# Optimization experiments

Hardware: AMD Instinct MI355X
Metric: run time of the kernel (lower is better)

Reference implementation:

```python
import jax, jax.numpy as jnp
import numpy as np

EMB = 300; TOWERS = 6; LAYERS = 4; EPS = 1e-5; F_OUT = EMB // TOWERS  # 50
N_NODES = 3000; N_EDGES = 9000; N_GRAPHS = 64
NODE_VOCAB = 16; EDGE_VOCAB = 4


def _bn(x, g, b, m, v):
    # eval-mode BatchNorm1d with running stats
    return (x - m) * jax.lax.rsqrt(v + EPS) * g + b


def _forward(node_emb, edge_emb, W_edge, b_edge, W_pre, b_pre, W_post, b_post,
             W_lin, b_lin, bn_gamma, bn_beta, bn_mean, bn_var,
             head_w0, head_b0, gn0_gamma, gn0_beta, gn0_mean, gn0_var,
             head_w1, head_b1, gn1_gamma, gn1_beta, gn1_mean, gn1_var,
             head_w2, head_b2, x, edge_index, edge_attr, batch, num_graphs):
    N = x.shape[0]
    src, dst = edge_index[0], edge_index[1]
    h = node_emb[x]            # [N, D] node encoder (categorical embedding)
    e = edge_emb[edge_attr]    # [E, D] edge encoder
    cnt = jax.ops.segment_sum(jnp.ones(src.shape, h.dtype), dst, num_segments=N)
    deg = jnp.maximum(cnt, 1.0)
    log_deg = jnp.log(deg + 1.0)
    avg_log = jnp.mean(jnp.log(cnt + 1.0))  # PNA avg_deg['log'] of degree histogram
    amp = (log_deg / avg_log)[:, None, None]
    att = (avg_log / log_deg)[:, None, None]
    has_nb = (cnt > 0)[:, None, None]
    degc = deg[:, None, None]

    h_list = [h]
    for l in range(LAYERS):
        eproj = e @ W_edge[l] + b_edge[l]                        # [E, D]
        hcat = jnp.concatenate([h[dst], h[src], eproj], -1)      # [E, 3D] = [x_i, x_j, e]
        m = jnp.einsum('ef,tfd->etd', hcat, W_pre[l]) + b_pre[l]  # [E, T, D] per-tower pre-MLP
        s = jax.ops.segment_sum(m, dst, num_segments=N)
        mean = s / degc
        mn = jnp.where(has_nb, jax.ops.segment_min(m, dst, num_segments=N), 0.0)
        mx = jnp.where(has_nb, jax.ops.segment_max(m, dst, num_segments=N), 0.0)
        var = jax.ops.segment_sum(m * m, dst, num_segments=N) / degc - mean * mean
        std = jnp.sqrt(jax.nn.relu(var) + EPS)
        agg = jnp.concatenate([mean, mn, mx, std], -1)           # [N, T, 4D]
        agg = jnp.concatenate([agg, agg * amp, agg * att], -1)   # [N, T, 12D] scalers
        x_rep = jnp.broadcast_to(h[:, None, :], (N, TOWERS, EMB))
        post_in = jnp.concatenate([x_rep, agg], -1)              # [N, T, 13D]
        out = jnp.einsum('ntf,tfo->nto', post_in, W_post[l]) + b_post[l]  # [N, T, F_OUT]
        out = out.reshape(N, EMB) @ W_lin[l] + b_lin[l]
        out = _bn(out, bn_gamma[l], bn_beta[l], bn_mean[l], bn_var[l])
        if l < LAYERS - 1:
            out = jax.nn.relu(out)  # dropout is identity in eval mode
        h_list.append(out)
        h = out
    # JK='sum' exactly as in the original forward: sums h_list[0..num_layer-1]
    node_rep = h_list[0]
    for l in range(1, LAYERS):
        node_rep = node_rep + h_list[l]
    g = jax.ops.segment_sum(node_rep, batch, num_segments=num_graphs)  # global_add_pool
    g = jax.nn.relu(_bn(g @ head_w0 + head_b0, gn0_gamma, gn0_beta, gn0_mean, gn0_var))
    g = jax.nn.relu(_bn(g @ head_w1 + head_b1, gn1_gamma, gn1_beta, gn1_mean, gn1_var))
    return g @ head_w2 + head_b2


def setup_inputs() -> dict:
    key = jax.random.key(0)
    ks = jax.random.split(key, 16)
    D, T, L = EMB, TOWERS, LAYERS
    def rn(k, shape, s=0.05):
        return jax.random.normal(k, shape, dtype=jnp.float32) * s
    return {
        'x': jax.random.randint(ks[0], (N_NODES,), 0, NODE_VOCAB, dtype=jnp.int32),
        'edge_index': jax.random.randint(ks[1], (2, N_EDGES), 0, N_NODES, dtype=jnp.int32),
        'edge_attr': jax.random.randint(ks[2], (N_EDGES,), 0, EDGE_VOCAB, dtype=jnp.int32),
        'batch': jnp.sort(jax.random.randint(ks[3], (N_NODES,), 0, N_GRAPHS, dtype=jnp.int32)),
        'num_graphs': N_GRAPHS,
        'node_emb': rn(ks[4], (NODE_VOCAB, D), 1.0),
        'edge_emb': rn(ks[5], (EDGE_VOCAB, D), 1.0),
        'W_edge': rn(ks[6], (L, D, D)), 'b_edge': jnp.zeros((L, D), jnp.float32),
        'W_pre': rn(ks[7], (L, T, 3 * D, D)), 'b_pre': jnp.zeros((L, T, D), jnp.float32),
        'W_post': rn(ks[8], (L, T, 13 * D, F_OUT)), 'b_post': jnp.zeros((L, T, F_OUT), jnp.float32),
        'W_lin': rn(ks[9], (L, D, D)), 'b_lin': jnp.zeros((L, D), jnp.float32),
        'bn_gamma': jnp.ones((L, D), jnp.float32), 'bn_beta': jnp.zeros((L, D), jnp.float32),
        'bn_mean': jnp.zeros((L, D), jnp.float32), 'bn_var': jnp.ones((L, D), jnp.float32),
        'head_w0': rn(ks[10], (D, 2 * D)), 'head_b0': jnp.zeros((2 * D,), jnp.float32),
        'gn0_gamma': jnp.ones((2 * D,), jnp.float32), 'gn0_beta': jnp.zeros((2 * D,), jnp.float32),
        'gn0_mean': jnp.zeros((2 * D,), jnp.float32), 'gn0_var': jnp.ones((2 * D,), jnp.float32),
        'head_w1': rn(ks[11], (2 * D, D)), 'head_b1': jnp.zeros((D,), jnp.float32),
        'gn1_gamma': jnp.ones((D,), jnp.float32), 'gn1_beta': jnp.zeros((D,), jnp.float32),
        'gn1_mean': jnp.zeros((D,), jnp.float32), 'gn1_var': jnp.ones((D,), jnp.float32),
        'head_w2': rn(ks[12], (D, 1)), 'head_b2': jnp.zeros((1,), jnp.float32),
    }


def reference(x, edge_index, edge_attr, batch, num_graphs,
              node_emb, edge_emb, W_edge, b_edge, W_pre, b_pre, W_post, b_post,
              W_lin, b_lin, bn_gamma, bn_beta, bn_mean, bn_var,
              head_w0, head_b0, gn0_gamma, gn0_beta, gn0_mean, gn0_var,
              head_w1, head_b1, gn1_gamma, gn1_beta, gn1_mean, gn1_var,
              head_w2, head_b2):
    return _forward(node_emb, edge_emb, W_edge, b_edge, W_pre, b_pre, W_post, b_post,
                    W_lin, b_lin, bn_gamma, bn_beta, bn_mean, bn_var,
                    head_w0, head_b0, gn0_gamma, gn0_beta, gn0_mean, gn0_var,
                    head_w1, head_b1, gn1_gamma, gn1_beta, gn1_mean, gn1_var,
                    head_w2, head_b2, x, edge_index, edge_attr, batch, num_graphs)
```

## Files before the change

### kernel.cpp

```cpp
#include <hip/hip_runtime.h>
#include <math.h>

#define NN 3000
#define NE 9000
#define NG 64
#define D 300
#define NT 6
#define FO 50
#define EPSV 1e-5f
#define NB1 3900

__global__ void k_hist(const int* __restrict__ dst, int* __restrict__ cnt) {
    int e = blockIdx.x * blockDim.x + threadIdx.x;
    if (e < NE) atomicAdd(&cnt[dst[e]], 1);
}

__global__ __launch_bounds__(1024) void k_scan(
    const int* __restrict__ cnt, int* __restrict__ row_ptr, int* __restrict__ tmp_ptr,
    float* __restrict__ degf, float* __restrict__ ampv, float* __restrict__ attv) {
    __shared__ int s_part[1024];
    __shared__ float s_log[1024];
    int tid = threadIdx.x;
    int base = tid * 3;
    int c0 = 0, c1 = 0, c2 = 0; float lg = 0.f;
    if (base + 0 < NN) { c0 = cnt[base + 0]; lg += logf((float)c0 + 1.f); }
    if (base + 1 < NN) { c1 = cnt[base + 1]; lg += logf((float)c1 + 1.f); }
    if (base + 2 < NN) { c2 = cnt[base + 2]; lg += logf((float)c2 + 1.f); }
    s_part[tid] = c0 + c1 + c2;
    s_log[tid] = lg;
    __syncthreads();
    for (int off = 1; off < 1024; off <<= 1) {
        int v = (tid >= off) ? s_part[tid - off] : 0;
        __syncthreads();
        s_part[tid] += v;
        __syncthreads();
    }
    for (int off = 512; off > 0; off >>= 1) {
        if (tid < off) s_log[tid] += s_log[tid + off];
        __syncthreads();
    }
    float avg = s_log[0] / (float)NN;
    int run = (tid > 0) ? s_part[tid - 1] : 0;
    int cs[3] = {c0, c1, c2};
    for (int i = 0; i < 3; i++) {
        int n = base + i;
        if (n < NN) {
            row_ptr[n] = run; tmp_ptr[n] = run;
            int cc = cs[i];
            float dd = (float)(cc > 0 ? cc : 1);
            degf[n] = dd;
            float ld = logf(dd + 1.f);
            ampv[n] = ld / avg;
            attv[n] = avg / ld;
            run += cc;
        }
    }
    if (tid == 1023) row_ptr[NN] = s_part[1023];
}

__global__ void k_fill(const int* __restrict__ src, const int* __restrict__ dst,
                       const int* __restrict__ attr, int* __restrict__ tmp_ptr,
                       int2* __restrict__ edge_dat) {
    int e = blockIdx.x * blockDim.x + threadIdx.x;
    if (e < NE) {
        int d = dst[e];
        int p = atomicAdd(&tmp_ptr[d], 1);
        edge_dat[p] = make_int2(src[e], attr[e]);
    }
}

__global__ void k_embed(const int* __restrict__ x, const float* __restrict__ node_emb,
                        float* __restrict__ h, float* __restrict__ rep) {
    int i = blockIdx.x * blockDim.x + threadIdx.x;
    if (i < NN * D) {
        int n = i / D, d = i - n * D;
        float v = node_emb[x[n] * D + d];
        h[i] = v; rep[i] = v;
    }
}

__global__ void k_pack1(const float* __restrict__ W_pre, const float* __restrict__ W_post,
                        int l, float* __restrict__ Bp) {
    int idx = blockIdx.x * blockDim.x + threadIdx.x;
    if (idx >= 300 * NB1) return;
    int f = idx / NB1, j = idx - f * NB1;
    float v;
    if (j < 3600) {
        int s = j / 1800, r = j - s * 1800;
        int t = r / 300, d = r - t * 300;
        v = W_pre[(((size_t)(l * NT + t) * 900) + s * 300 + f) * 300 + d];
    } else {
        int jj = j - 3600;
        int t = jj / FO, o = jj - t * FO;
        v = W_post[((size_t)(l * NT + t) * 3900 + f) * FO + o];
    }
    Bp[idx] = v;
}

__global__ void k_packpost(const float* __restrict__ W_post, int l, float* __restrict__ Bp) {
    int idx = blockIdx.x * blockDim.x + threadIdx.x;
    if (idx >= NT * 1200 * 160) return;
    int t = idx / 192000, r = idx - t * 192000;
    int f = r / 160, c = r - f * 160;
    float v = 0.f;
    if (c < 150) {
        int k = c / FO, o = c - k * FO;
        v = W_post[((size_t)(l * NT + t) * 3900 + 300 + k * 1200 + f) * FO + o];
    }
    Bp[idx] = v;
}

__global__ void k_ep4(const float* __restrict__ edge_emb, const float* __restrict__ W_edge,
                      const float* __restrict__ b_edge, int l, float* __restrict__ ep4) {
    int idx = blockIdx.x * blockDim.x + threadIdx.x;
    if (idx >= 4 * 300) return;
    int a = idx / 300, f = idx - a * 300;
    float s = b_edge[l * 300 + f];
    for (int k = 0; k < 300; k++)
        s = fmaf(edge_emb[a * 300 + k], W_edge[((size_t)l * 300 + k) * 300 + f], s);
    ep4[idx] = s;
}

__global__ void k_ep_proj(const float* __restrict__ ep4, const float* __restrict__ W_pre,
                          const float* __restrict__ b_pre, int l, float* __restrict__ Ep) {
    int idx = blockIdx.x * blockDim.x + threadIdx.x;
    if (idx >= 4 * 1800) return;
    int a = idx / 1800, c = idx - a * 1800;
    int t = c / 300, d = c - t * 300;
    float s = b_pre[(l * NT + t) * 300 + d];
    for (int f = 0; f < 300; f++)
        s = fmaf(ep4[a * 300 + f], W_pre[(((size_t)(l * NT + t) * 900) + 600 + f) * 300 + d], s);
    Ep[idx] = s;
}

__global__ void k_pack_lin(const float* __restrict__ W_lin, const float* __restrict__ b_lin,
                           const float* __restrict__ gam, const float* __restrict__ bet,
                           const float* __restrict__ mu, const float* __restrict__ var,
                           int l, float* __restrict__ Wf, float* __restrict__ bf) {
    int idx = blockIdx.x * blockDim.x + threadIdx.x;
    if (idx >= 300 * 300) return;
    int f = idx / 300, j = idx - f * 300;
    float s = gam[l * 300 + j] * rsqrtf(var[l * 300 + j] + EPSV);
    Wf[idx] = W_lin[((size_t)l * 300 + f) * 300 + j] * s;
    if (f == 0) bf[j] = (b_lin[l * 300 + j] - mu[l * 300 + j]) * s + bet[l * 300 + j];
}

template <int EPI>
__global__ __launch_bounds__(256) void k_gemm(
    const float* __restrict__ A, int lda,
    const float* __restrict__ B, int ldb,
    float* __restrict__ C, int ldc,
    int M, int N, int K,
    const float* __restrict__ bias, float* __restrict__ rep,
    const float* __restrict__ gam, const float* __restrict__ bet,
    const float* __restrict__ mu, const float* __restrict__ var) {
    constexpr int BM = 64, BN = 64, BK = 16, LAS = BM + 4;
    __shared__ float As[BK * LAS];
    __shared__ float Bs[BK * BN];
    int tid = threadIdx.x;
    int tx = tid & 15, ty = tid >> 4;
    int bm = blockIdx.y * BM, bn = blockIdx.x * BN;
    int arow = tid >> 2;
    int akq = (tid & 3) * 4;
    int bj = tid & 63, bk0 = tid >> 6;
    float acc[4][4] = {};
    for (int k0 = 0; k0 < K; k0 += BK) {
        {
            float4 av = make_float4(0.f, 0.f, 0.f, 0.f);
            int grow = bm + arow;
            if (grow < M) {
                int gk = k0 + akq;
                if (gk + 3 < K) {
                    av = *(const float4*)&A[(size_t)grow * lda + gk];
                } else {
                    float t0 = (gk + 0 < K) ? A[(size_t)grow * lda + gk + 0] : 0.f;
                    float t1 = (gk + 1 < K) ? A[(size_t)grow * lda + gk + 1] : 0.f;
                    float t2 = (gk + 2 < K) ? A[(size_t)grow * lda + gk + 2] : 0.f;
                    float t3 = (gk + 3 < K) ? A[(size_t)grow * lda + gk + 3] : 0.f;
                    av = make_float4(t0, t1, t2, t3);
                }
            }
            As[(akq + 0) * LAS + arow] = av.x;
            As[(akq + 1) * LAS + arow] = av.y;
            As[(akq + 2) * LAS + arow] = av.z;
            As[(akq + 3) * LAS + arow] = av.w;
        }
        #pragma unroll
        for (int it = 0; it < 4; ++it) {
            int k = bk0 + it * 4;
            int gk = k0 + k, gj = bn + bj;
            float v = 0.f;
            if (gk < K && gj < N) v = B[(size_t)gk * ldb + gj];
            Bs[k * BN + bj] = v;
        }
        __syncthreads();
        #pragma unroll
        for (int kk = 0; kk < BK; ++kk) {
            float4 a = *(const float4*)&As[kk * LAS + ty * 4];
            float4 b = *(const float4*)&Bs[kk * BN + tx * 4];
            float ar[4] = {a.x, a.y, a.z, a.w};
            float br[4] = {b.x, b.y, b.z, b.w};
            #pragma unroll
            for (int i = 0; i < 4; i++)
                #pragma unroll
                for (int j = 0; j < 4; j++)
                    acc[i][j] = fmaf(ar[i], br[j], acc[i][j]);
        }
        __syncthreads();
    }
    #pragma unroll
    for (int i = 0; i < 4; i++) {
        int r = bm + ty * 4 + i;
        if (r >= M) continue;
        #pragma unroll
        for (int j = 0; j < 4; j++) {
            int c = bn + tx * 4 + j;
            if (c >= N) continue;
            float v = acc[i][j];
            if (EPI == 1) {
                v += bias[c];
                v = fmaxf(v, 0.f);
                C[(size_t)r * ldc + c] = v;
                rep[(size_t)r * ldc + c] += v;
            } else if (EPI == 2) {
                v += bias[c];
                v = (v - mu[c]) * rsqrtf(var[c] + EPSV) * gam[c] + bet[c];
                v = fmaxf(v, 0.f);
                C[(size_t)r * ldc + c] = v;
            } else {
                C[(size_t)r * ldc + c] = v;
            }
        }
    }
}

__global__ __launch_bounds__(256) void k_gemm1(const float* __restrict__ A,
                                               const float* __restrict__ B,
                                               float* __restrict__ C) {
    constexpr int BM = 128, BN = 128, BK = 16, LAS = BM + 4;
    constexpr int M = 3000, N = NB1, K = 300;
    __shared__ float As[BK * LAS];
    __shared__ float Bs[BK * BN];
    int tid = threadIdx.x;
    int tx = tid & 15, ty = tid >> 4;
    int bm = blockIdx.y * BM, bn = blockIdx.x * BN;
    float acc[8][8] = {};
    for (int k0 = 0; k0 < K; k0 += BK) {
        #pragma unroll
        for (int it = 0; it < 2; ++it) {
            int i = tid + it * 256;
            int row = i >> 2, kq = (i & 3) * 4;
            int grow = bm + row, gk = k0 + kq;
            float4 av = make_float4(0.f, 0.f, 0.f, 0.f);
            if (grow < M && gk < K) av = *(const float4*)&A[(size_t)grow * 300 + gk];
            As[(kq + 0) * LAS + row] = av.x;
            As[(kq + 1) * LAS + row] = av.y;
            As[(kq + 2) * LAS + row] = av.z;
            As[(kq + 3) * LAS + row] = av.w;
        }
        #pragma unroll
        for (int it = 0; it < 2; ++it) {
            int i = tid + it * 256;
            int k = i >> 5, c = (i & 31) * 4;
            int gk = k0 + k, gj = bn + c;
            float4 bv = make_float4(0.f, 0.f, 0.f, 0.f);
            if (gk < K && gj < N) bv = *(const float4*)&B[(size_t)gk * N + gj];
            *(float4*)&Bs[k * BN + c] = bv;
        }
        __syncthreads();
        #pragma unroll
        for (int kk = 0; kk < BK; ++kk) {
            float a[8], b[8];
            *(float4*)&a[0] = *(const float4*)&As[kk * LAS + ty * 8];
            *(float4*)&a[4] = *(const float4*)&As[kk * LAS + ty * 8 + 4];
            *(float4*)&b[0] = *(const float4*)&Bs[kk * BN + tx * 8];
            *(float4*)&b[4] = *(const float4*)&Bs[kk * BN + tx * 8 + 4];
            #pragma unroll
            for (int i = 0; i < 8; i++)
                #pragma unroll
                for (int j = 0; j < 8; j++)
                    acc[i][j] = fmaf(a[i], b[j], acc[i][j]);
        }
        __syncthreads();
    }
    int r0 = bm + ty * 8, c0 = bn + tx * 8;
    #pragma unroll
    for (int i = 0; i < 8; i++) {
        int r = r0 + i;
        if (r >= M) break;
        if (c0 + 8 <= N) {
            float4 v0 = make_float4(acc[i][0], acc[i][1], acc[i][2], acc[i][3]);
            float4 v1 = make_float4(acc[i][4], acc[i][5], acc[i][6], acc[i][7]);
            *(float4*)&C[(size_t)r * N + c0] = v0;
            *(float4*)&C[(size_t)r * N + c0 + 4] = v1;
        } else {
            #pragma unroll
            for (int j = 0; j < 8; j++)
                if (c0 + j < N) C[(size_t)r * N + c0 + j] = acc[i][j];
        }
    }
}

__global__ __launch_bounds__(256) void k_gemmp(const float* __restrict__ agg,
                                               const float* __restrict__ Bp,
                                               float* __restrict__ P) {
    constexpr int BM = 64, BN = 160, BK = 16, LAS = BM + 4, KC = 240;
    __shared__ float As[BK * LAS];
    __shared__ float Bs[BK * BN];
    int z = blockIdx.z;
    int t = z % 6, kc = z / 6;
    const float* A = agg + t * 1200 + kc * KC;
    const float* B = Bp + t * 192000 + kc * KC * 160;
    float* C = P + (size_t)z * 480000;
    int tid = threadIdx.x;
    int tx = tid & 15, ty = tid >> 4;
    int bm = blockIdx.y * BM;
    float acc[4][10] = {};
    for (int k0 = 0; k0 < KC; k0 += BK) {
        {
            int row = tid >> 2, kq = (tid & 3) * 4;
            int grow = bm + row;
            float4 av = make_float4(0.f, 0.f, 0.f, 0.f);
            if (grow < 3000) av = *(const float4*)&A[(size_t)grow * 7200 + k0 + kq];
            As[(kq + 0) * LAS + row] = av.x;
            As[(kq + 1) * LAS + row] = av.y;
            As[(kq + 2) * LAS + row] = av.z;
            As[(kq + 3) * LAS + row] = av.w;
        }
        #pragma unroll
        for (int it = 0; it < 3; ++it) {
            int i = tid + it * 256;
            if (i < 640) {
                int k = i / 40, c = (i - k * 40) * 4;
                *(float4*)&Bs[k * BN + c] = *(const float4*)&B[(size_t)(k0 + k) * 160 + c];
            }
        }
        __syncthreads();
        #pragma unroll
        for (int kk = 0; kk < BK; ++kk) {
            float a[4], b[10];
            *(float4*)&a[0] = *(const float4*)&As[kk * LAS + ty * 4];
            #pragma unroll
            for (int j = 0; j < 10; j++) b[j] = Bs[kk * BN + tx * 10 + j];
            #pragma unroll
            for (int i = 0; i < 4; i++)
                #pragma unroll
                for (int j = 0; j < 10; j++)
                    acc[i][j] = fmaf(a[i], b[j], acc[i][j]);
        }
        __syncthreads();
    }
    int r0 = bm + ty * 4, c0 = tx * 10;
    #pragma unroll
    for (int i = 0; i < 4; i++) {
        int r = r0 + i;
        if (r >= 3000) break;
        #pragma unroll
        for (int j = 0; j < 10; j++)
            C[(size_t)r * 160 + c0 + j] = acc[i][j];
    }
}

__global__ __launch_bounds__(256) void k_agg(
    const float* __restrict__ HH, const float* __restrict__ Ep,
    const int* __restrict__ row_ptr, const int2* __restrict__ edge_dat,
    const float* __restrict__ degf, const int* __restrict__ xv, int use_vocab,
    float* __restrict__ agg) {
    int n = blockIdx.x;
    int e0 = row_ptr[n], e1 = row_ptr[n + 1];
    int cnt = e1 - e0;
    float cntf = (float)cnt;
    float deg = degf[n];
    float inv_deg = 1.f / deg;
    int nrow = use_vocab ? xv[n] : n;
    const float* hdrow = HH + (size_t)nrow * NB1;
    for (int c4 = threadIdx.x; c4 < 450; c4 += 256) {
        int c = c4 * 4;
        float sx = 0.f, sy = 0.f, sz = 0.f, sw = 0.f;
        float qx = 0.f, qy = 0.f, qz = 0.f, qw = 0.f;
        float mnx = INFINITY, mny = INFINITY, mnz = INFINITY, mnw = INFINITY;
        float mxx = -INFINITY, mxy = -INFINITY, mxz = -INFINITY, mxw = -INFINITY;
        for (int e = e0; e < e1; ++e) {
            int2 sa = edge_dat[e];
            int srow = use_vocab ? xv[sa.x] : sa.x;
            float4 hv = *(const float4*)&HH[(size_t)srow * NB1 + 1800 + c];
            float4 ev = *(const float4*)&Ep[(size_t)sa.y * 1800 + c];
            float vx = hv.x + ev.x, vy = hv.y + ev.y, vz = hv.z + ev.z, vw = hv.w + ev.w;
            sx += vx; sy += vy; sz += vz; sw += vw;
            qx = fmaf(vx, vx, qx); qy = fmaf(vy, vy, qy);
            qz = fmaf(vz, vz, qz); qw = fmaf(vw, vw, qw);
            mnx = fminf(mnx, vx); mny = fminf(mny, vy);
            mnz = fminf(mnz, vz); mnw = fminf(mnw, vw);
            mxx = fmaxf(mxx, vx); mxy = fmaxf(mxy, vy);
            mxz = fmaxf(mxz, vz); mxw = fmaxf(mxw, vw);
        }
        float4 hd = *(const float4*)&hdrow[c];
        float4 mean, mnv, mxv, stdv;
        {
            mean.x = (cntf * hd.x + sx) * inv_deg;
            mean.y = (cntf * hd.y + sy) * inv_deg;
            mean.z = (cntf * hd.z + sz) * inv_deg;
            mean.w = (cntf * hd.w + sw) * inv_deg;
            if (cnt > 0) {
                mnv.x = hd.x + mnx; mnv.y = hd.y + mny; mnv.z = hd.z + mnz; mnv.w = hd.w + mnw;
                mxv.x = hd.x + mxx; mxv.y = hd.y + mxy; mxv.z = hd.z + mxz; mxv.w = hd.w + mxw;
            } else {
                mnv = make_float4(0.f, 0.f, 0.f, 0.f);
                mxv = make_float4(0.f, 0.f, 0.f, 0.f);
            }
            float vrx = (cntf * hd.x * hd.x + 2.f * hd.x * sx + qx) * inv_deg - mean.x * mean.x;
            float vry = (cntf * hd.y * hd.y + 2.f * hd.y * sy + qy) * inv_deg - mean.y * mean.y;
            float vrz = (cntf * hd.z * hd.z + 2.f * hd.z * sz + qz) * inv_deg - mean.z * mean.z;
            float vrw = (cntf * hd.w * hd.w + 2.f * hd.w * sw + qw) * inv_deg - mean.w * mean.w;
            stdv.x = sqrtf(fmaxf(vrx, 0.f) + EPSV);
            stdv.y = sqrtf(fmaxf(vry, 0.f) + EPSV);
            stdv.z = sqrtf(fmaxf(vrz, 0.f) + EPSV);
            stdv.w = sqrtf(fmaxf(vrw, 0.f) + EPSV);
        }
        int t = c / 300, d = c - t * 300;
        float* arow = agg + (size_t)n * 7200 + (size_t)t * 1200 + d;
        *(float4*)&arow[0]   = mean;
        *(float4*)&arow[300] = mnv;
        *(float4*)&arow[600] = mxv;
        *(float4*)&arow[900] = stdv;
    }
}

__global__ void k_combine(const float* __restrict__ HH, const float* __restrict__ P,
                          const float* __restrict__ ampv, const float* __restrict__ attv,
                          const float* __restrict__ b_post_l, const int* __restrict__ xv,
                          int use_vocab, float* __restrict__ out_pre) {
    int i = blockIdx.x * blockDim.x + threadIdx.x;
    if (i >= NN * D) return;
    int n = i / D, j = i - n * D;
    int t = j / FO, o = j - t * FO;
    int nrow = use_vocab ? xv[n] : n;
    float p1 = 0.f, p2 = 0.f, p3 = 0.f;
    #pragma unroll
    for (int kc = 0; kc < 5; kc++) {
        const float* Pr = P + ((size_t)(kc * 6 + t) * 3000 + n) * 160;
        p1 += Pr[o];
        p2 += Pr[50 + o];
        p3 += Pr[100 + o];
    }
    float v = HH[(size_t)nrow * NB1 + 3600 + j] + p1 + ampv[n] * p2 + attv[n] * p3
              + b_post_l[t * FO + o];
    out_pre[i] = v;
}

__global__ __launch_bounds__(256) void k_pool(const float* __restrict__ rep,
                                              const int* __restrict__ batch,
                                              float* __restrict__ g) {
    __shared__ int s_lo, s_hi;
    int b = blockIdx.x;
    if (threadIdx.x == 0) {
        int lo = 0, hi = NN;
        while (lo < hi) { int m = (lo + hi) >> 1; if (batch[m] < b) lo = m + 1; else hi = m; }
        s_lo = lo;
        int lo2 = lo, hi2 = NN;
        while (lo2 < hi2) { int m = (lo2 + hi2) >> 1; if (batch[m] < b + 1) lo2 = m + 1; else hi2 = m; }
        s_hi = lo2;
    }
    __syncthreads();
    int lo = s_lo, hi = s_hi;
    for (int j = threadIdx.x; j < D; j += blockDim.x) {
        float s = 0.f;
        for (int n = lo; n < hi; ++n) s += rep[(size_t)n * D + j];
        g[b * D + j] = s;
    }
}

__global__ void k_head2(const float* __restrict__ g2, const float* __restrict__ w2,
                        const float* __restrict__ b2, float* __restrict__ out) {
    int b = blockIdx.x;
    int tid = threadIdx.x;
    float s = 0.f;
    for (int k = tid; k < 300; k += 64) s += g2[b * 300 + k] * w2[k];
    for (int off = 32; off; off >>= 1) s += __shfl_down(s, off, 64);
    if (tid == 0) out[b] = s + b2[0];
}

extern "C" void kernel_launch(void* const* d_in, const int* in_sizes, int n_in,
                              void* d_out, int out_size, void* d_ws, size_t ws_size,
                              hipStream_t stream) {
    const int* x      = (const int*)d_in[0];
    const int* ei     = (const int*)d_in[1];
    const int* src    = ei;
    const int* dst    = ei + NE;
    const int* eattr  = (const int*)d_in[2];
    const int* batch  = (const int*)d_in[3];
    const float* node_emb = (const float*)d_in[5];
    const float* edge_emb = (const float*)d_in[6];
    const float* W_edge   = (const float*)d_in[7];
    const float* b_edge   = (const float*)d_in[8];
    const float* W_pre    = (const float*)d_in[9];
    const float* b_pre    = (const float*)d_in[10];
    const float* W_post   = (const float*)d_in[11];
    const float* b_post   = (const float*)d_in[12];
    const float* W_lin    = (const float*)d_in[13];
    const float* b_lin    = (const float*)d_in[14];
    const float* bn_gamma = (const float*)d_in[15];
    const float* bn_beta  = (const float*)d_in[16];
    const float* bn_mean  = (const float*)d_in[17];
    const float* bn_var   = (const float*)d_in[18];
    const float* head_w0  = (const float*)d_in[19];
    const float* head_b0  = (const float*)d_in[20];
    const float* gn0_g    = (const float*)d_in[21];
    const float* gn0_b    = (const float*)d_in[22];
    const float* gn0_m    = (const float*)d_in[23];
    const float* gn0_v    = (const float*)d_in[24];
    const float* head_w1  = (const float*)d_in[25];
    const float* head_b1  = (const float*)d_in[26];
    const float* gn1_g    = (const float*)d_in[27];
    const float* gn1_b    = (const float*)d_in[28];
    const float* gn1_m    = (const float*)d_in[29];
    const float* gn1_v    = (const float*)d_in[30];
    const float* head_w2  = (const float*)d_in[31];
    const float* head_b2  = (const float*)d_in[32];
    float* out = (float*)d_out;

    unsigned char* base = (unsigned char*)d_ws;
    size_t off = 0;
    auto alloc = [&](size_t bytes) -> void* {
        void* p = base + off;
        off += (bytes + 255) & ~(size_t)255;
        return p;
    };
    int*   cnt      = (int*)alloc(NN * 4);
    int*   row_ptr  = (int*)alloc((NN + 1) * 4);
    int*   tmp_ptr  = (int*)alloc(NN * 4);
    int2*  edge_dat = (int2*)alloc(NE * 8);
    float* degf     = (float*)alloc(NN * 4);
    float* ampv     = (float*)alloc(NN * 4);
    float* attv     = (float*)alloc(NN * 4);
    float* h        = (float*)alloc((size_t)NN * D * 4);
    float* rep      = (float*)alloc((size_t)NN * D * 4);
    float* HsHd     = (float*)alloc((size_t)NN * NB1 * 4);
    float* Bpack1   = (float*)alloc((size_t)300 * NB1 * 4);
    float* ep4      = (float*)alloc(4 * 300 * 4);
    float* Ep       = (float*)alloc(4 * 1800 * 4);
    float* agg      = (float*)alloc((size_t)NN * 7200 * 4);
    float* Bpost    = (float*)alloc((size_t)NT * 1200 * 160 * 4);
    float* P        = (float*)alloc((size_t)30 * 3000 * 160 * 4);
    float* out_pre  = (float*)alloc((size_t)NN * D * 4);
    float* Wlin_f   = (float*)alloc((size_t)300 * 300 * 4);
    float* b_f      = (float*)alloc(300 * 4);
    float* gsum     = (float*)alloc(NG * D * 4);
    float* gbuf0    = (float*)alloc(NG * 600 * 4);
    float* gbuf1    = (float*)alloc(NG * 300 * 4);
    (void)ws_size; (void)n_in; (void)in_sizes; (void)out_size;

    hipMemsetAsync(cnt, 0, NN * 4, stream);
    k_hist<<<(NE + 255) / 256, 256, 0, stream>>>(dst, cnt);
    k_scan<<<1, 1024, 0, stream>>>(cnt, row_ptr, tmp_ptr, degf, ampv, attv);
    k_fill<<<(NE + 255) / 256, 256, 0, stream>>>(src, dst, eattr, tmp_ptr, edge_dat);
    k_embed<<<(NN * D + 255) / 256, 256, 0, stream>>>(x, node_emb, h, rep);

    for (int l = 0; l < 3; ++l) {
        const float* Ain = (l == 0) ? node_emb : h;
        int M = (l == 0) ? 16 : NN;
        int uv = (l == 0) ? 1 : 0;

        k_pack1<<<(300 * NB1 + 255) / 256, 256, 0, stream>>>(W_pre, W_post, l, Bpack1);
        if (l == 0) {
            k_gemm<0><<<dim3((NB1 + 63) / 64, 1, 1), 256, 0, stream>>>(
                Ain, 300, Bpack1, NB1, HsHd, NB1, M, NB1, 300,
                nullptr, nullptr, nullptr, nullptr, nullptr, nullptr);
        } else {
            k_gemm1<<<dim3((NB1 + 127) / 128, 24, 1), 256, 0, stream>>>(Ain, Bpack1, HsHd);
        }

        k_ep4<<<(1200 + 255) / 256, 256, 0, stream>>>(edge_emb, W_edge, b_edge, l, ep4);
        k_ep_proj<<<(7200 + 255) / 256, 256, 0, stream>>>(ep4, W_pre, b_pre, l, Ep);

        k_agg<<<NN, 256, 0, stream>>>(HsHd, Ep, row_ptr, edge_dat, degf, x, uv, agg);

        k_packpost<<<(NT * 1200 * 160 + 255) / 256, 256, 0, stream>>>(W_post, l, Bpost);
        k_gemmp<<<dim3(1, 47, 30), 256, 0, stream>>>(agg, Bpost, P);

        k_combine<<<(NN * D + 255) / 256, 256, 0, stream>>>(
            HsHd, P, ampv, attv, b_post + l * NT * FO, x, uv, out_pre);

        k_pack_lin<<<(300 * 300 + 255) / 256, 256, 0, stream>>>(
            W_lin, b_lin, bn_gamma, bn_beta, bn_mean, bn_var, l, Wlin_f, b_f);
        k_gemm<1><<<dim3(5, 47, 1), 256, 0, stream>>>(
            out_pre, 300, Wlin_f, 300, h, 300, NN, 300, 300,
            b_f, rep, nullptr, nullptr, nullptr, nullptr);
    }

    k_pool<<<NG, 256, 0, stream>>>(rep, batch, gsum);
    k_gemm<2><<<dim3(10, 1, 1), 256, 0, stream>>>(
        gsum, 300, head_w0, 600, gbuf0, 600, NG, 600, 300,
        head_b0, nullptr, gn0_g, gn0_b, gn0_m, gn0_v);
    k_gemm<2><<<dim3(5, 1, 1), 256, 0, stream>>>(
        gbuf0, 600, head_w1, 300, gbuf1, 300, NG, 300, 600,
        head_b1, nullptr, gn1_g, gn1_b, gn1_m, gn1_v);
    k_head2<<<NG, 64, 0, stream>>>(gbuf1, head_w2, head_b2, out);
}
```

Measured before the change: 1.343 ms.

## Replace FP32 SIMT GEMM with split-bf16 MFMA GEMM for node projections

```diff
diff --git a/kernel.cpp b/kernel.cpp
--- a/kernel.cpp
+++ b/kernel.cpp
@@ -1,4 +1,5 @@
 #include <hip/hip_runtime.h>
+#include <hip/hip_bf16.h>
 #include <math.h>
 
 #define NN 3000
@@ -9,6 +10,21 @@
 #define FO 50
 #define EPSV 1e-5f
 #define NB1 3900
+#define MP 3008
+#define NP 3904
+#define KP 320
+
+typedef __attribute__((ext_vector_type(8))) short short8;
+typedef __attribute__((ext_vector_type(4))) float floatx4;
+
+__device__ inline unsigned short f2bf_rne(float f) {
+    unsigned u = __float_as_uint(f);
+    unsigned r = (u + 0x7FFF + ((u >> 16) & 1)) >> 16;
+    return (unsigned short)r;
+}
+__device__ inline float bf2f(unsigned short h) {
+    return __uint_as_float((unsigned)h << 16);
+}
 
 __global__ void k_hist(const int* __restrict__ dst, int* __restrict__ cnt) {
     int e = blockIdx.x * blockDim.x + threadIdx.x;
@@ -95,6 +111,41 @@
         v = W_post[((size_t)(l * NT + t) * 3900 + f) * FO + o];
     }
     Bp[idx] = v;
+}
+
+__global__ void k_pack1b(const float* __restrict__ W_pre, const float* __restrict__ W_post,
+                         int l, unsigned short* __restrict__ Bh, unsigned short* __restrict__ Bl) {
+    int idx = blockIdx.x * blockDim.x + threadIdx.x;
+    if (idx >= (KP / 8) * NP * 8) return;
+    int kb = idx / (NP * 8), r = idx - kb * NP * 8;
+    int n = r / 8, j = r - n * 8;
+    int k = kb * 8 + j;
+    float v = 0.f;
+    if (k < 300 && n < NB1) {
+        if (n < 3600) {
+            int s = n / 1800, rr = n - s * 1800;
+            int t = rr / 300, d = rr - t * 300;
+            v = W_pre[(((size_t)(l * NT + t) * 900) + s * 300 + k) * 300 + d];
+        } else {
+            int jj = n - 3600;
+            int t = jj / FO, o = jj - t * FO;
+            v = W_post[((size_t)(l * NT + t) * 3900 + k) * FO + o];
+        }
+    }
+    unsigned short hi = f2bf_rne(v);
+    Bh[idx] = hi;
+    Bl[idx] = f2bf_rne(v - bf2f(hi));
+}
+
+__global__ void k_splitA(const float* __restrict__ A, unsigned short* __restrict__ Ah,
+                         unsigned short* __restrict__ Al) {
+    int i = blockIdx.x * blockDim.x + threadIdx.x;
+    if (i >= MP * KP) return;
+    int n = i / KP, k = i - n * KP;
+    float v = (n < NN && k < 300) ? A[n * 300 + k] : 0.f;
+    unsigned short hi = f2bf_rne(v);
+    Ah[i] = hi;
+    Al[i] = f2bf_rne(v - bf2f(hi));
 }
 
 __global__ void k_packpost(const float* __restrict__ W_post, int l, float* __restrict__ Bp) {
@@ -234,69 +285,60 @@
     }
 }
 
-__global__ __launch_bounds__(256) void k_gemm1(const float* __restrict__ A,
-                                               const float* __restrict__ B,
-                                               float* __restrict__ C) {
-    constexpr int BM = 128, BN = 128, BK = 16, LAS = BM + 4;
-    constexpr int M = 3000, N = NB1, K = 300;
-    __shared__ float As[BK * LAS];
-    __shared__ float Bs[BK * BN];
+__global__ __launch_bounds__(256) void k_gemm1m(
+    const unsigned short* __restrict__ Ah, const unsigned short* __restrict__ Al,
+    const unsigned short* __restrict__ Bh, const unsigned short* __restrict__ Bl,
+    float* __restrict__ C) {
     int tid = threadIdx.x;
-    int tx = tid & 15, ty = tid >> 4;
-    int bm = blockIdx.y * BM, bn = blockIdx.x * BN;
-    float acc[8][8] = {};
-    for (int k0 = 0; k0 < K; k0 += BK) {
+    int wave = tid >> 6, lane = tid & 63;
+    int wr = wave >> 1, wc = wave & 1;
+    int lr = lane & 15, lg = lane >> 4;
+    int row0 = blockIdx.y * 64 + wr * 32;
+    int col0 = blockIdx.x * 64 + wc * 32;
+    floatx4 acc00 = {0.f, 0.f, 0.f, 0.f}, acc01 = {0.f, 0.f, 0.f, 0.f};
+    floatx4 acc10 = {0.f, 0.f, 0.f, 0.f}, acc11 = {0.f, 0.f, 0.f, 0.f};
+    const unsigned short* paH = Ah + (size_t)(row0 + lr) * KP + lg * 8;
+    const unsigned short* paL = Al + (size_t)(row0 + lr) * KP + lg * 8;
+    const unsigned short* pbH = Bh + ((size_t)lg * NP + col0 + lr) * 8;
+    const unsigned short* pbL = Bl + ((size_t)lg * NP + col0 + lr) * 8;
+    #pragma unroll
+    for (int ks = 0; ks < KP / 32; ++ks) {
+        int ao = ks * 32;
+        size_t bo = (size_t)ks * 4 * NP * 8;
+        short8 ah0 = *(const short8*)(paH + ao);
+        short8 ah1 = *(const short8*)(paH + 16 * KP + ao);
+        short8 al0 = *(const short8*)(paL + ao);
+        short8 al1 = *(const short8*)(paL + 16 * KP + ao);
+        short8 bh0 = *(const short8*)(pbH + bo);
+        short8 bh1 = *(const short8*)(pbH + bo + 128);
+        short8 bl0 = *(const short8*)(pbL + bo);
+        short8 bl1 = *(const short8*)(pbL + bo + 128);
+        acc00 = __builtin_amdgcn_mfma_f32_16x16x32_bf16(ah0, bh0, acc00, 0, 0, 0);
+        acc01 = __builtin_amdgcn_mfma_f32_16x16x32_bf16(ah0, bh1, acc01, 0, 0, 0);
+        acc10 = __builtin_amdgcn_mfma_f32_16x16x32_bf16(ah1, bh0, acc10, 0, 0, 0);
+        acc11 = __builtin_amdgcn_mfma_f32_16x16x32_bf16(ah1, bh1, acc11, 0, 0, 0);
+        acc00 = __builtin_amdgcn_mfma_f32_16x16x32_bf16(ah0, bl0, acc00, 0, 0, 0);
+        acc01 = __builtin_amdgcn_mfma_f32_16x16x32_bf16(ah0, bl1, acc01, 0, 0, 0);
+        acc10 = __builtin_amdgcn_mfma_f32_16x16x32_bf16(ah1, bl0, acc10, 0, 0, 0);
+        acc11 = __builtin_amdgcn_mfma_f32_16x16x32_bf16(ah1, bl1, acc11, 0, 0, 0);
+        acc00 = __builtin_amdgcn_mfma_f32_16x16x32_bf16(al0, bh0, acc00, 0, 0, 0);
+        acc01 = __builtin_amdgcn_mfma_f32_16x16x32_bf16(al0, bh1, acc01, 0, 0, 0);
+        acc10 = __builtin_amdgcn_mfma_f32_16x16x32_bf16(al1, bh0, acc10, 0, 0, 0);
+        acc11 = __builtin_amdgcn_mfma_f32_16x16x32_bf16(al1, bh1, acc11, 0, 0, 0);
+    }
+    #pragma unroll
+    for (int i = 0; i < 2; i++) {
         #pragma unroll
-        for (int it = 0; it < 2; ++it) {
-            int i = tid + it * 256;
-            int row = i >> 2, kq = (i & 3) * 4;
-            int grow = bm + row, gk = k0 + kq;
-            float4 av = make_float4(0.f, 0.f, 0.f, 0.f);
-            if (grow < M && gk < K) av = *(const float4*)&A[(size_t)grow * 300 + gk];
-            As[(kq + 0) * LAS + row] = av.x;
-            As[(kq + 1) * LAS + row] = av.y;
-            As[(kq + 2) * LAS + row] = av.z;
-            As[(kq + 3) * LAS + row] = av.w;
-        }
-        #pragma unroll
-        for (int it = 0; it < 2; ++it) {
-            int i = tid + it * 256;
-            int k = i >> 5, c = (i & 31) * 4;
-            int gk = k0 + k, gj = bn + c;
-            float4 bv = make_float4(0.f, 0.f, 0.f, 0.f);
-            if (gk < K && gj < N) bv = *(const float4*)&B[(size_t)gk * N + gj];
-            *(float4*)&Bs[k * BN + c] = bv;
-        }
-        __syncthreads();
-        #pragma unroll
-        for (int kk = 0; kk < BK; ++kk) {
-            float a[8], b[8];
-            *(float4*)&a[0] = *(const float4*)&As[kk * LAS + ty * 8];
-            *(float4*)&a[4] = *(const float4*)&As[kk * LAS + ty * 8 + 4];
-            *(float4*)&b[0] = *(const float4*)&Bs[kk * BN + tx * 8];
-            *(float4*)&b[4] = *(const float4*)&Bs[kk * BN + tx * 8 + 4];
+        for (int j = 0; j < 2; j++) {
+            floatx4 a = (i == 0) ? ((j == 0) ? acc00 : acc01)
+                                 : ((j == 0) ? acc10 : acc11);
+            int col = col0 + j * 16 + lr;
             #pragma unroll
-            for (int i = 0; i < 8; i++)
-                #pragma unroll
-                for (int j = 0; j < 8; j++)
-                    acc[i][j] = fmaf(a[i], b[j], acc[i][j]);
-        }
-        __syncthreads();
-    }
-    int r0 = bm + ty * 8, c0 = bn + tx * 8;
-    #pragma unroll
-    for (int i = 0; i < 8; i++) {
-        int r = r0 + i;
-        if (r >= M) break;
-        if (c0 + 8 <= N) {
-            float4 v0 = make_float4(acc[i][0], acc[i][1], acc[i][2], acc[i][3]);
-            float4 v1 = make_float4(acc[i][4], acc[i][5], acc[i][6], acc[i][7]);
-            *(float4*)&C[(size_t)r * N + c0] = v0;
-            *(float4*)&C[(size_t)r * N + c0 + 4] = v1;
-        } else {
-            #pragma unroll
-            for (int j = 0; j < 8; j++)
-                if (c0 + j < N) C[(size_t)r * N + c0 + j] = acc[i][j];
+            for (int r = 0; r < 4; r++) {
+                int row = row0 + i * 16 + lg * 4 + r;
+                if (row < NN && col < NB1)
+                    C[(size_t)row * NB1 + col] = a[r];
+            }
         }
     }
 }
@@ -537,6 +579,10 @@
     float* rep      = (float*)alloc((size_t)NN * D * 4);
     float* HsHd     = (float*)alloc((size_t)NN * NB1 * 4);
     float* Bpack1   = (float*)alloc((size_t)300 * NB1 * 4);
+    unsigned short* Ah = (unsigned short*)alloc((size_t)MP * KP * 2);
+    unsigned short* Al = (unsigned short*)alloc((size_t)MP * KP * 2);
+    unsigned short* Bh = (unsigned short*)alloc((size_t)(KP / 8) * NP * 8 * 2);
+    unsigned short* Bl = (unsigned short*)alloc((size_t)(KP / 8) * NP * 8 * 2);
     float* ep4      = (float*)alloc(4 * 300 * 4);
     float* Ep       = (float*)alloc(4 * 1800 * 4);
     float* agg      = (float*)alloc((size_t)NN * 7200 * 4);
@@ -561,13 +607,16 @@
         int M = (l == 0) ? 16 : NN;
         int uv = (l == 0) ? 1 : 0;
 
-        k_pack1<<<(300 * NB1 + 255) / 256, 256, 0, stream>>>(W_pre, W_post, l, Bpack1);
         if (l == 0) {
+            k_pack1<<<(300 * NB1 + 255) / 256, 256, 0, stream>>>(W_pre, W_post, l, Bpack1);
             k_gemm<0><<<dim3((NB1 + 63) / 64, 1, 1), 256, 0, stream>>>(
                 Ain, 300, Bpack1, NB1, HsHd, NB1, M, NB1, 300,
                 nullptr, nullptr, nullptr, nullptr, nullptr, nullptr);
         } else {
-            k_gemm1<<<dim3((NB1 + 127) / 128, 24, 1), 256, 0, stream>>>(Ain, Bpack1, HsHd);
+            k_splitA<<<(MP * KP + 255) / 256, 256, 0, stream>>>(h, Ah, Al);
+            k_pack1b<<<((KP / 8) * NP * 8 + 255) / 256, 256, 0, stream>>>(
+                W_pre, W_post, l, Bh, Bl);
+            k_gemm1m<<<dim3(NP / 64, MP / 64, 1), 256, 0, stream>>>(Ah, Al, Bh, Bl, HsHd);
         }
 
         k_ep4<<<(1200 + 255) / 256, 256, 0, stream>>>(edge_emb, W_edge, b_edge, l, ep4);
```

Result: faster. 1.286 ms (-4.3%).
